# Performance work log

Measured on AMD Instinct MI355X. Metric: run time of the kernel, lower is better.

Reference implementation:

```python
import jax, jax.numpy as jnp
import numpy as np
import math

BOUND = 1e-06
PI = math.pi

N_DIMS = 256
N_ROWS = 524288
DELTA = 1e-06


def _make_buffers(n_dims, delta, radius, scaling, range_type="bound"):
    if range_type == "whole":
        phi_L = 0.0
    else:  # 'bound'
        L = 0.01
        upper_bound = PI / 2 * (1.0 - L)
        phi_L = math.asin(delta ** (1.0 / n_dims))
        phi_L = phi_L if phi_L < upper_bound else upper_bound
    # W_theta: identity with last row duplicated -> (n_dims+1, n_dims)
    eye = np.eye(n_dims, dtype=np.float32)
    W_theta = np.concatenate([eye, eye[-1:]], axis=0)
    # W_phi: strictly upper-triangular ones, with [-2, -1] zeroed
    W_phi = np.triu(np.ones((n_dims + 1, n_dims + 1), dtype=np.float32), k=1)
    W_phi[-2, -1] = 0.0
    b_phi = np.zeros(n_dims + 1, dtype=np.float32)
    b_phi[-1] = -PI / 2.0
    return (
        jnp.float32(phi_L),
        jnp.asarray(W_theta),
        jnp.asarray(W_phi),
        jnp.asarray(b_phi),
        jnp.float32(radius),
        jnp.float32(scaling),
    )


def setup_inputs() -> dict:
    key = jax.random.key(0)
    x = jax.random.normal(key, (N_ROWS, N_DIMS), dtype=jnp.float32)
    phi_L, W_theta, W_phi, b_phi, radius, scaling = _make_buffers(
        N_DIMS, DELTA, radius=1.0, scaling=1.0, range_type="bound"
    )
    return {
        "x": x,
        "W_theta": W_theta,
        "W_phi": W_phi,
        "b_phi": b_phi,
        "phi_L": phi_L,
        "radius": radius,
        "scaling": scaling,
    }


def reference(x, W_theta, W_phi, b_phi, phi_L, radius, scaling):
    # Map features to angles in [phi_L, pi/2)
    ang = (PI / 2 - phi_L) * jax.nn.sigmoid(scaling * x) + phi_L
    # Duplicate last angle: [N, n_dims] -> [N, n_dims+1]
    a = jnp.matmul(ang, W_theta.T)
    # log-sin cumulative sum (via strictly-upper-triangular matmul) + log-cos term
    logx = jnp.matmul(jnp.log(jnp.sin(a) + BOUND), W_phi) + jnp.log(
        jnp.cos(a + b_phi) + BOUND
    )
    return radius * jnp.exp(logx)
```

## Files before the change

kernel.cpp:

```cpp
#include <hip/hip_runtime.h>

#define BOUND 1e-6f
#define HALF_PI 1.57079632679489662f
#define LOG2E 1.44269504088896341f

#define UPD_DPP(oldv, srcv, ctrl, rmask)                                        \
  __int_as_float(__builtin_amdgcn_update_dpp(                                   \
      __float_as_int(oldv), __float_as_int(srcv), (ctrl), (rmask), 0xF, false))

__device__ __forceinline__ float wave_incl_prod(float x) {
    x *= UPD_DPP(1.0f, x, 0x111, 0xF);
    x *= UPD_DPP(1.0f, x, 0x112, 0xF);
    x *= UPD_DPP(1.0f, x, 0x114, 0xF);
    x *= UPD_DPP(1.0f, x, 0x118, 0xF);
    x *= UPD_DPP(1.0f, x, 0x142, 0xA);
    x *= UPD_DPP(1.0f, x, 0x143, 0xC);
    return x;
}

__global__ __launch_bounds__(256) void spherize_kernel(
    const float* __restrict__ x,
    const float* __restrict__ p_phiL,
    const float* __restrict__ p_radius,
    const float* __restrict__ p_scaling,
    float* __restrict__ out,
    int n_rows, int n_groups, int total_waves)
{
    __shared__ float lds[4 * 1028];

    const float phi_L  = p_phiL[0];
    const float radius = p_radius[0];
    const float cexp   = p_scaling[0] * LOG2E;
    const float amp    = HALF_PI - phi_L;

    const int lane = threadIdx.x & 63;
    const int wave = threadIdx.x >> 6;
    float* myl = lds + wave * 1028;

    auto LOADG = [&](float4 (&r)[4], int g) {
        const int r0 = g * 4;
        const float* xb = x + (size_t)r0 * 256 + lane * 4;
        #pragma unroll
        for (int i = 0; i < 4; ++i)
            if (r0 + i < n_rows)
                r[i] = *reinterpret_cast<const float4*>(xb + i * 256);
    };

    auto PROC = [&](const float4 (&r)[4], int g) {
        const int r0 = g * 4;
        const int nr = min(4, n_rows - r0);
        #pragma unroll
        for (int i = 0; i < 4; ++i) {
            if (i >= nr) break;
            const float* xp = &r[i].x;
            float s[4], cc[4];
            #pragma unroll
            for (int k = 0; k < 4; ++k) {
                float e  = __builtin_amdgcn_exp2f(cexp * xp[k]);
                float u  = amp * __builtin_amdgcn_rcpf(1.0f + e);
                float u2 = u * u;
                s[k] = fmaf(u2, fmaf(u2, 4.16666667e-2f, -0.5f), 1.0f + BOUND);
                float p = fmaf(u2, fmaf(u2, 8.33333333e-3f, -1.66666667e-1f), 1.0f);
                cc[k] = fmaf(u, p, BOUND);
            }
            float q1 = s[0];
            float q2 = q1 * s[1];
            float q3 = q2 * s[2];
            float t  = q3 * s[3];
            float scan = wave_incl_prod(t);
            float excl = UPD_DPP(1.0f, scan, 0x138, 0xF);
            float base = radius * excl;

            float* lrow = myl + i * 257 + lane * 4;
            lrow[0] = base * cc[0];
            lrow[1] = base * q1 * cc[1];
            lrow[2] = base * q2 * cc[2];
            lrow[3] = base * q3 * cc[3];
            if (lane == 63)
                lrow[4] = radius * scan;
        }
        asm volatile("s_waitcnt lgkmcnt(0)" ::: "memory");

        float* obase = out + (size_t)r0 * 257;
        if (nr == 4) {
            const float4* l4 = reinterpret_cast<const float4*>(myl);
            float4*       o4 = reinterpret_cast<float4*>(obase);
            o4[lane]       = l4[lane];
            o4[lane + 64]  = l4[lane + 64];
            o4[lane + 128] = l4[lane + 128];
            o4[lane + 192] = l4[lane + 192];
            if (lane == 0) o4[256] = l4[256];
        } else {
            const int nd = nr * 257;
            for (int j = lane; j < nd; j += 64) obase[j] = myl[j];
        }
    };

    int g = blockIdx.x * 4 + wave;
    if (g >= n_groups) return;

    float4 A[4], B[4];
    LOADG(A, g);
    for (;;) {
        const int g1 = g + total_waves;
        if (g1 < n_groups) LOADG(B, g1);
        PROC(A, g);
        if (g1 >= n_groups) break;
        const int g2 = g1 + total_waves;
        if (g2 < n_groups) LOADG(A, g2);
        PROC(B, g1);
        if (g2 >= n_groups) break;
        g = g2;
    }
}

extern "C" void kernel_launch(void* const* d_in, const int* in_sizes, int n_in,
                              void* d_out, int out_size, void* d_ws, size_t ws_size,
                              hipStream_t stream) {
    const float* x         = (const float*)d_in[0];
    const float* p_phiL    = (const float*)d_in[4];
    const float* p_radius  = (const float*)d_in[5];
    const float* p_scaling = (const float*)d_in[6];
    float* out = (float*)d_out;

    const int n_rows   = in_sizes[0] / 256;
    const int n_groups = (n_rows + 3) / 4;
    int blocks = 2048;
    if (blocks * 4 > n_groups) blocks = (n_groups + 3) / 4;
    const int total_waves = blocks * 4;

    spherize_kernel<<<blocks, 256, 0, stream>>>(x, p_phiL, p_radius, p_scaling,
                                                out, n_rows, n_groups, total_waves);
}
```

Before: 216.4 us.

## Replace persistent grid-stride loop with one-shot blocks of 16 contiguous rows per wave

```diff
diff --git a/kernel.cpp b/kernel.cpp
--- a/kernel.cpp
+++ b/kernel.cpp
@@ -24,7 +24,7 @@
     const float* __restrict__ p_radius,
     const float* __restrict__ p_scaling,
     float* __restrict__ out,
-    int n_rows, int n_groups, int total_waves)
+    int n_rows)
 {
     __shared__ float lds[4 * 1028];
 
@@ -37,8 +37,11 @@
     const int wave = threadIdx.x >> 6;
     float* myl = lds + wave * 1028;
 
+    const int wrow0 = (blockIdx.x * 4 + wave) * 16;
+    if (wrow0 >= n_rows) return;
+
     auto LOADG = [&](float4 (&r)[4], int g) {
-        const int r0 = g * 4;
+        const int r0 = wrow0 + g * 4;
         const float* xb = x + (size_t)r0 * 256 + lane * 4;
         #pragma unroll
         for (int i = 0; i < 4; ++i)
@@ -47,8 +50,9 @@
     };
 
     auto PROC = [&](const float4 (&r)[4], int g) {
-        const int r0 = g * 4;
+        const int r0 = wrow0 + g * 4;
         const int nr = min(4, n_rows - r0);
+        if (nr <= 0) return;
         #pragma unroll
         for (int i = 0; i < 4; ++i) {
             if (i >= nr) break;
@@ -96,22 +100,12 @@
         }
     };
 
-    int g = blockIdx.x * 4 + wave;
-    if (g >= n_groups) return;
-
     float4 A[4], B[4];
-    LOADG(A, g);
-    for (;;) {
-        const int g1 = g + total_waves;
-        if (g1 < n_groups) LOADG(B, g1);
-        PROC(A, g);
-        if (g1 >= n_groups) break;
-        const int g2 = g1 + total_waves;
-        if (g2 < n_groups) LOADG(A, g2);
-        PROC(B, g1);
-        if (g2 >= n_groups) break;
-        g = g2;
-    }
+    LOADG(A, 0);
+    LOADG(B, 1); PROC(A, 0);
+    LOADG(A, 2); PROC(B, 1);
+    LOADG(B, 3); PROC(A, 2);
+    PROC(B, 3);
 }
 
 extern "C" void kernel_launch(void* const* d_in, const int* in_sizes, int n_in,
@@ -123,12 +117,9 @@
     const float* p_scaling = (const float*)d_in[6];
     float* out = (float*)d_out;
 
-    const int n_rows   = in_sizes[0] / 256;
-    const int n_groups = (n_rows + 3) / 4;
-    int blocks = 2048;
-    if (blocks * 4 > n_groups) blocks = (n_groups + 3) / 4;
-    const int total_waves = blocks * 4;
+    const int n_rows = in_sizes[0] / 256;
+    const int blocks = (n_rows + 63) / 64;
 
     spherize_kernel<<<blocks, 256, 0, stream>>>(x, p_phiL, p_radius, p_scaling,
-                                                out, n_rows, n_groups, total_waves);
+                                                out, n_rows);
 }
```

New measurement: 217.7 us. About the same (+0.6%).
